# Kernel optimization log

Measured on AMD Instinct MI355X. Metric: run time of the kernel, lower is better.

Reference implementation:

```python
import jax, jax.numpy as jnp
import numpy as np

N = 100_000      # nodes
E = 1_600_000    # directed edges (avg degree 16)
IN_C, HID, LAT, L = 128, 64, 32, 3


def setup_inputs() -> dict:
    key = jax.random.key(0)
    ks = jax.random.split(key, 12)
    s = 0.05
    x = jax.random.normal(ks[0], (N, IN_C), dtype=jnp.float32)
    edge_index = jax.random.randint(ks[1], (2, E), 0, N, dtype=jnp.int32)
    W_in = jax.random.normal(ks[2], (IN_C, HID), dtype=jnp.float32) * s
    b_in = jnp.zeros((HID,), jnp.float32)
    Wg = jax.random.normal(ks[3], (L, HID, HID), dtype=jnp.float32) * s
    bg = jnp.zeros((L, HID), jnp.float32)
    Ws = jax.random.normal(ks[4], (L, HID, LAT), dtype=jnp.float32) * s
    bs = jnp.zeros((L, LAT), jnp.float32)
    Wl = jax.random.normal(ks[5], (HID, LAT), dtype=jnp.float32) * s
    bl = jnp.zeros((LAT,), jnp.float32)
    return {"x": x, "edge_index": edge_index, "W_in": W_in, "b_in": b_in,
            "Wg": Wg, "bg": bg, "Ws": Ws, "bs": bs, "Wl": Wl, "bl": bl}


def reference(x, edge_index, W_in, b_in, Wg, bg, Ws, bs, Wl, bl):
    # --- GCN normalization (PyG GCNConv: add self-loops, sym deg norm) ---
    src, dst = edge_index[0], edge_index[1]
    loops = jnp.arange(N, dtype=src.dtype)
    src_f = jnp.concatenate([src, loops])   # [E+N]
    dst_f = jnp.concatenate([dst, loops])
    deg = jax.ops.segment_sum(jnp.ones(E + N, x.dtype), dst_f, num_segments=N)
    dinv = jnp.where(deg > 0, jax.lax.rsqrt(deg), 0.0)
    norm = (dinv[src_f] * dinv[dst_f])[:, None]  # [E+N, 1]

    def gcn(h, W, b):
        hw = h @ W                                   # [N, out]
        msg = hw[src_f] * norm                       # gather + scale
        return jax.ops.segment_sum(msg, dst_f, num_segments=N) + b

    h = x @ W_in + b_in
    skips = []
    for i in range(L):
        skips.append(h)
        h = jax.nn.leaky_relu(gcn(h, Wg[i], bg[i]), negative_slope=0.2)
        # dropout(p=0.01) is identity in eval mode
    latent = gcn(h, Wl, bl)
    for i in range(L):
        latent = latent + skips[i] @ Ws[i] + bs[i]
    return latent
```

## Files before the change

kernel.cpp:

```cpp
#include <hip/hip_runtime.h>


#define HID 64
#define LAT 32
#define PW 128

static inline int cdiv(long long a, long long b) { return (int)((a + b - 1) / b); }


__global__ __launch_bounds__(256) void hist_kernel(const int* __restrict__ dst,
                                                   int* __restrict__ hist,
                                                   int E, int nb1, int chunk) {
    __shared__ int h[1024];
    int w = blockIdx.x, t = threadIdx.x;
    for (int i = t; i < nb1; i += 256) h[i] = 0;
    __syncthreads();
    int beg = w * chunk, end = min(E, beg + chunk);
    for (int e = beg + t; e < end; e += 256) atomicAdd(&h[dst[e] >> 7], 1);
    __syncthreads();
    for (int i = t; i < nb1; i += 256) hist[i * PW + w] = h[i];
}

__global__ __launch_bounds__(PW) void colscan_kernel(const int* __restrict__ hist,
                                                     int* __restrict__ colprefix,
                                                     int* __restrict__ btot) {
    __shared__ int s[PW];
    int b = blockIdx.x, t = threadIdx.x;
    int v = hist[b * PW + t];
    s[t] = v;
    __syncthreads();
    for (int off = 1; off < PW; off <<= 1) {
        int x = (t >= off) ? s[t - off] : 0;
        __syncthreads();
        s[t] += x;
        __syncthreads();
    }
    colprefix[b * PW + t] = s[t] - v;
    if (t == PW - 1) btot[b] = s[t];
}

__global__ __launch_bounds__(1024) void bscan_kernel(const int* __restrict__ btot,
                                                     int* __restrict__ bstart, int nb1, int E) {
    __shared__ int s[1024];
    int t = threadIdx.x;
    int v = (t < nb1) ? btot[t] : 0;
    s[t] = v;
    __syncthreads();
    for (int off = 1; off < 1024; off <<= 1) {
        int x = (t >= off) ? s[t - off] : 0;
        __syncthreads();
        s[t] += x;
        __syncthreads();
    }
    if (t < nb1) bstart[t] = s[t] - v;
    if (t == 0) bstart[nb1] = E;
}

__global__ __launch_bounds__(256) void partition_kernel(
        const int* __restrict__ src, const int* __restrict__ dst,
        const int* __restrict__ bstart, const int* __restrict__ colprefix,
        unsigned* __restrict__ bbuf, int E, int nb1, int chunk) {
    __shared__ int cur[1024];
    int w = blockIdx.x, t = threadIdx.x;
    for (int i = t; i < nb1; i += 256) cur[i] = bstart[i] + colprefix[i * PW + w];
    __syncthreads();
    int beg = w * chunk, end = min(E, beg + chunk);
    for (int e = beg + t; e < end; e += 256) {
        int s = src[e], d = dst[e];
        int pos = atomicAdd(&cur[d >> 7], 1);
        bbuf[pos] = ((unsigned)(d & 127) << 17) | (unsigned)s;
    }
}

__global__ __launch_bounds__(256) void build_csr_kernel(
        const int* __restrict__ bstart, const unsigned* __restrict__ bbuf,
        int* __restrict__ csr, int* __restrict__ rowstart, float* __restrict__ dinv,
        int n, int E) {
    __shared__ int lcount[128], lpre[128], lcur[128];
    int b = blockIdx.x, t = threadIdx.x;
    int bst = bstart[b], bend = bstart[b + 1];

    if (t < 128) lcount[t] = 0;
    __syncthreads();
    for (int i = bst + t; i < bend; i += 256) atomicAdd(&lcount[bbuf[i] >> 17], 1);
    __syncthreads();
    if (t == 0) {
        int run = 0;
        for (int k = 0; k < 128; ++k) {
            lpre[k] = run;
            lcur[k] = run;
            run += lcount[k];
        }
    }
    __syncthreads();
    if (t < 128) {
        int v = (b << 7) + t;
        if (v < n) {
            rowstart[v] = bst + lpre[t];
            dinv[v] = rsqrtf((float)(lcount[t] + 1));
        }
    }
    if (b == 0 && t == 0) rowstart[n] = E;
    for (int i = bst + t; i < bend; i += 256) {
        unsigned p = bbuf[i];
        int pos = bst + atomicAdd(&lcur[p >> 17], 1);
        csr[pos] = (int)(p & 0x1FFFFu);
    }
}


__global__ __launch_bounds__(256) void input_fused_kernel(
        const float* __restrict__ x, const float* __restrict__ Win,
        const float* __restrict__ bin, const float* __restrict__ Wg0,
        const float* __restrict__ Ws0, const float* __restrict__ dinv,
        const float* __restrict__ bl, const float* __restrict__ bs,
        float* __restrict__ hw, float* __restrict__ out, int n) {
    __shared__ float h0[64 * 68];
    int t = threadIdx.x;
    int vbase = blockIdx.x * 64;
    int rg = t >> 4, lc = t & 15;

    int r0 = vbase + rg * 4;
    const float* xp0 = x + (size_t)(r0 + 0 < n ? r0 + 0 : n - 1) * 128;
    const float* xp1 = x + (size_t)(r0 + 1 < n ? r0 + 1 : n - 1) * 128;
    const float* xp2 = x + (size_t)(r0 + 2 < n ? r0 + 2 : n - 1) * 128;
    const float* xp3 = x + (size_t)(r0 + 3 < n ? r0 + 3 : n - 1) * 128;

    {
        float4 b4 = *(const float4*)&bin[4 * lc];
        float4 a0 = b4, a1 = b4, a2 = b4, a3 = b4;
#pragma unroll 4
        for (int k = 0; k < 128; k += 4) {
            float4 x0 = *(const float4*)&xp0[k];
            float4 x1 = *(const float4*)&xp1[k];
            float4 x2 = *(const float4*)&xp2[k];
            float4 x3 = *(const float4*)&xp3[k];
            float4 w;
            w = *(const float4*)&Win[(k + 0) * 64 + 4 * lc];
            a0.x = fmaf(x0.x, w.x, a0.x); a0.y = fmaf(x0.x, w.y, a0.y);
            a0.z = fmaf(x0.x, w.z, a0.z); a0.w = fmaf(x0.x, w.w, a0.w);
            a1.x = fmaf(x1.x, w.x, a1.x); a1.y = fmaf(x1.x, w.y, a1.y);
            a1.z = fmaf(x1.x, w.z, a1.z); a1.w = fmaf(x1.x, w.w, a1.w);
            a2.x = fmaf(x2.x, w.x, a2.x); a2.y = fmaf(x2.x, w.y, a2.y);
            a2.z = fmaf(x2.x, w.z, a2.z); a2.w = fmaf(x2.x, w.w, a2.w);
            a3.x = fmaf(x3.x, w.x, a3.x); a3.y = fmaf(x3.x, w.y, a3.y);
            a3.z = fmaf(x3.x, w.z, a3.z); a3.w = fmaf(x3.x, w.w, a3.w);
            w = *(const float4*)&Win[(k + 1) * 64 + 4 * lc];
            a0.x = fmaf(x0.y, w.x, a0.x); a0.y = fmaf(x0.y, w.y, a0.y);
            a0.z = fmaf(x0.y, w.z, a0.z); a0.w = fmaf(x0.y, w.w, a0.w);
            a1.x = fmaf(x1.y, w.x, a1.x); a1.y = fmaf(x1.y, w.y, a1.y);
            a1.z = fmaf(x1.y, w.z, a1.z); a1.w = fmaf(x1.y, w.w, a1.w);
            a2.x = fmaf(x2.y, w.x, a2.x); a2.y = fmaf(x2.y, w.y, a2.y);
            a2.z = fmaf(x2.y, w.z, a2.z); a2.w = fmaf(x2.y, w.w, a2.w);
            a3.x = fmaf(x3.y, w.x, a3.x); a3.y = fmaf(x3.y, w.y, a3.y);
            a3.z = fmaf(x3.y, w.z, a3.z); a3.w = fmaf(x3.y, w.w, a3.w);
            w = *(const float4*)&Win[(k + 2) * 64 + 4 * lc];
            a0.x = fmaf(x0.z, w.x, a0.x); a0.y = fmaf(x0.z, w.y, a0.y);
            a0.z = fmaf(x0.z, w.z, a0.z); a0.w = fmaf(x0.z, w.w, a0.w);
            a1.x = fmaf(x1.z, w.x, a1.x); a1.y = fmaf(x1.z, w.y, a1.y);
            a1.z = fmaf(x1.z, w.z, a1.z); a1.w = fmaf(x1.z, w.w, a1.w);
            a2.x = fmaf(x2.z, w.x, a2.x); a2.y = fmaf(x2.z, w.y, a2.y);
            a2.z = fmaf(x2.z, w.z, a2.z); a2.w = fmaf(x2.z, w.w, a2.w);
            a3.x = fmaf(x3.z, w.x, a3.x); a3.y = fmaf(x3.z, w.y, a3.y);
            a3.z = fmaf(x3.z, w.z, a3.z); a3.w = fmaf(x3.z, w.w, a3.w);
            w = *(const float4*)&Win[(k + 3) * 64 + 4 * lc];
            a0.x = fmaf(x0.w, w.x, a0.x); a0.y = fmaf(x0.w, w.y, a0.y);
            a0.z = fmaf(x0.w, w.z, a0.z); a0.w = fmaf(x0.w, w.w, a0.w);
            a1.x = fmaf(x1.w, w.x, a1.x); a1.y = fmaf(x1.w, w.y, a1.y);
            a1.z = fmaf(x1.w, w.z, a1.z); a1.w = fmaf(x1.w, w.w, a1.w);
            a2.x = fmaf(x2.w, w.x, a2.x); a2.y = fmaf(x2.w, w.y, a2.y);
            a2.z = fmaf(x2.w, w.z, a2.z); a2.w = fmaf(x2.w, w.w, a2.w);
            a3.x = fmaf(x3.w, w.x, a3.x); a3.y = fmaf(x3.w, w.y, a3.y);
            a3.z = fmaf(x3.w, w.z, a3.z); a3.w = fmaf(x3.w, w.w, a3.w);
        }
        *(float4*)&h0[(rg * 4 + 0) * 68 + 4 * lc] = a0;
        *(float4*)&h0[(rg * 4 + 1) * 68 + 4 * lc] = a1;
        *(float4*)&h0[(rg * 4 + 2) * 68 + 4 * lc] = a2;
        *(float4*)&h0[(rg * 4 + 3) * 68 + 4 * lc] = a3;
    }
    __syncthreads();

    {
        float4 a0, a1, a2, a3;
        a0 = a1 = a2 = a3 = make_float4(0.f, 0.f, 0.f, 0.f);
#pragma unroll 8
        for (int k = 0; k < 64; ++k) {
            float4 w = *(const float4*)&Wg0[k * 64 + 4 * lc];
            float x0 = h0[(rg * 4 + 0) * 68 + k];
            float x1 = h0[(rg * 4 + 1) * 68 + k];
            float x2 = h0[(rg * 4 + 2) * 68 + k];
            float x3 = h0[(rg * 4 + 3) * 68 + k];
            a0.x = fmaf(x0, w.x, a0.x); a0.y = fmaf(x0, w.y, a0.y);
            a0.z = fmaf(x0, w.z, a0.z); a0.w = fmaf(x0, w.w, a0.w);
            a1.x = fmaf(x1, w.x, a1.x); a1.y = fmaf(x1, w.y, a1.y);
            a1.z = fmaf(x1, w.z, a1.z); a1.w = fmaf(x1, w.w, a1.w);
            a2.x = fmaf(x2, w.x, a2.x); a2.y = fmaf(x2, w.y, a2.y);
            a2.z = fmaf(x2, w.z, a2.z); a2.w = fmaf(x2, w.w, a2.w);
            a3.x = fmaf(x3, w.x, a3.x); a3.y = fmaf(x3, w.y, a3.y);
            a3.z = fmaf(x3, w.z, a3.z); a3.w = fmaf(x3, w.w, a3.w);
        }
#pragma unroll
        for (int r = 0; r < 4; ++r) {
            int v = vbase + rg * 4 + r;
            if (v < n) {
                float di = dinv[v];
                float4 a = (r == 0) ? a0 : (r == 1) ? a1 : (r == 2) ? a2 : a3;
                a.x *= di; a.y *= di; a.z *= di; a.w *= di;
                *(float4*)&hw[(size_t)v * 64 + 4 * lc] = a;
            }
        }
    }

    {
        int sg = t >> 3, sc = t & 7;
        float4 bb = *(const float4*)&bl[4 * sc];
        float4 q0 = *(const float4*)&bs[4 * sc];
        float4 q1 = *(const float4*)&bs[LAT + 4 * sc];
        float4 q2 = *(const float4*)&bs[2 * LAT + 4 * sc];
        bb.x += q0.x + q1.x + q2.x; bb.y += q0.y + q1.y + q2.y;
        bb.z += q0.z + q1.z + q2.z; bb.w += q0.w + q1.w + q2.w;
        float4 a0 = bb, a1 = bb;
#pragma unroll 8
        for (int k = 0; k < 64; ++k) {
            float4 w = *(const float4*)&Ws0[k * 32 + 4 * sc];
            float x0 = h0[(sg * 2 + 0) * 68 + k];
            float x1 = h0[(sg * 2 + 1) * 68 + k];
            a0.x = fmaf(x0, w.x, a0.x); a0.y = fmaf(x0, w.y, a0.y);
            a0.z = fmaf(x0, w.z, a0.z); a0.w = fmaf(x0, w.w, a0.w);
            a1.x = fmaf(x1, w.x, a1.x); a1.y = fmaf(x1, w.y, a1.y);
            a1.z = fmaf(x1, w.z, a1.z); a1.w = fmaf(x1, w.w, a1.w);
        }
#pragma unroll
        for (int r = 0; r < 2; ++r) {
            int v = vbase + sg * 2 + r;
            if (v < n)
                *(float4*)&out[(size_t)v * 32 + 4 * sc] = (r == 0) ? a0 : a1;
        }
    }
}


template <bool LAST>
__global__ __launch_bounds__(256) void gather_transform_kernel(
        const int* __restrict__ rowstart, const int* __restrict__ csr,
        const float* __restrict__ dinv, const float* __restrict__ hwin,
        const float* __restrict__ bias, const float* __restrict__ Wg,
        const float* __restrict__ Ws, float* __restrict__ hwout,
        float* __restrict__ out, int n) {
    __shared__ float hL[64 * 68];
    int t = threadIdx.x;
    int vbase = blockIdx.x * 64;
    int ns = t >> 4, lc = t & 15;

    float4 b4 = *(const float4*)&bias[4 * lc];
#pragma unroll
    for (int b = 0; b < 4; ++b) {
        int row = b * 16 + ns;
        int v = vbase + row;
        if (v < n) {
            int beg = rowstart[v];
            int end = rowstart[v + 1];
            float di = dinv[v];
            float4 acc = *(const float4*)&hwin[(size_t)v * 64 + 4 * lc];
            const float* base = hwin + 4 * lc;
            int e = beg;
            for (; e + 3 < end; e += 4) {
                int s0 = csr[e], s1 = csr[e + 1], s2 = csr[e + 2], s3 = csr[e + 3];
                float4 g0 = *(const float4*)&base[(size_t)s0 * 64];
                float4 g1 = *(const float4*)&base[(size_t)s1 * 64];
                float4 g2 = *(const float4*)&base[(size_t)s2 * 64];
                float4 g3 = *(const float4*)&base[(size_t)s3 * 64];
                acc.x += (g0.x + g1.x) + (g2.x + g3.x);
                acc.y += (g0.y + g1.y) + (g2.y + g3.y);
                acc.z += (g0.z + g1.z) + (g2.z + g3.z);
                acc.w += (g0.w + g1.w) + (g2.w + g3.w);
            }
            for (; e < end; ++e) {
                float4 g0 = *(const float4*)&base[(size_t)csr[e] * 64];
                acc.x += g0.x; acc.y += g0.y; acc.z += g0.z; acc.w += g0.w;
            }
            float4 h;
            h.x = di * acc.x + b4.x; h.x = h.x > 0.f ? h.x : 0.2f * h.x;
            h.y = di * acc.y + b4.y; h.y = h.y > 0.f ? h.y : 0.2f * h.y;
            h.z = di * acc.z + b4.z; h.z = h.z > 0.f ? h.z : 0.2f * h.z;
            h.w = di * acc.w + b4.w; h.w = h.w > 0.f ? h.w : 0.2f * h.w;
            *(float4*)&hL[row * 68 + 4 * lc] = h;
        }
    }
    __syncthreads();

    if (!LAST) {
        int rg = t >> 4;
        float4 a0, a1, a2, a3;
        a0 = a1 = a2 = a3 = make_float4(0.f, 0.f, 0.f, 0.f);
#pragma unroll 8
        for (int k = 0; k < 64; ++k) {
            float4 w = *(const float4*)&Wg[k * 64 + 4 * lc];
            float x0 = hL[(rg * 4 + 0) * 68 + k];
            float x1 = hL[(rg * 4 + 1) * 68 + k];
            float x2 = hL[(rg * 4 + 2) * 68 + k];
            float x3 = hL[(rg * 4 + 3) * 68 + k];
            a0.x = fmaf(x0, w.x, a0.x); a0.y = fmaf(x0, w.y, a0.y);
            a0.z = fmaf(x0, w.z, a0.z); a0.w = fmaf(x0, w.w, a0.w);
            a1.x = fmaf(x1, w.x, a1.x); a1.y = fmaf(x1, w.y, a1.y);
            a1.z = fmaf(x1, w.z, a1.z); a1.w = fmaf(x1, w.w, a1.w);
            a2.x = fmaf(x2, w.x, a2.x); a2.y = fmaf(x2, w.y, a2.y);
            a2.z = fmaf(x2, w.z, a2.z); a2.w = fmaf(x2, w.w, a2.w);
            a3.x = fmaf(x3, w.x, a3.x); a3.y = fmaf(x3, w.y, a3.y);
            a3.z = fmaf(x3, w.z, a3.z); a3.w = fmaf(x3, w.w, a3.w);
        }
#pragma unroll
        for (int r = 0; r < 4; ++r) {
            int v = vbase + rg * 4 + r;
            if (v < n) {
                float di = dinv[v];
                float4 a = (r == 0) ? a0 : (r == 1) ? a1 : (r == 2) ? a2 : a3;
                a.x *= di; a.y *= di; a.z *= di; a.w *= di;
                *(float4*)&hwout[(size_t)v * 64 + 4 * lc] = a;
            }
        }

        int sg = t >> 3, sc = t & 7;
        float4 s0, s1;
        s0 = s1 = make_float4(0.f, 0.f, 0.f, 0.f);
#pragma unroll 8
        for (int k = 0; k < 64; ++k) {
            float4 w = *(const float4*)&Ws[k * 32 + 4 * sc];
            float x0 = hL[(sg * 2 + 0) * 68 + k];
            float x1 = hL[(sg * 2 + 1) * 68 + k];
            s0.x = fmaf(x0, w.x, s0.x); s0.y = fmaf(x0, w.y, s0.y);
            s0.z = fmaf(x0, w.z, s0.z); s0.w = fmaf(x0, w.w, s0.w);
            s1.x = fmaf(x1, w.x, s1.x); s1.y = fmaf(x1, w.y, s1.y);
            s1.z = fmaf(x1, w.z, s1.z); s1.w = fmaf(x1, w.w, s1.w);
        }
#pragma unroll
        for (int r = 0; r < 2; ++r) {
            int v = vbase + sg * 2 + r;
            if (v < n) {
                float4 a = (r == 0) ? s0 : s1;
                float4* op = (float4*)(out + (size_t)v * 32 + 4 * sc);
                float4 o = *op;
                o.x += a.x; o.y += a.y; o.z += a.z; o.w += a.w;
                *op = o;
            }
        }
    } else {
        int sg = t >> 3, sc = t & 7;
        float4 s0, s1;
        s0 = s1 = make_float4(0.f, 0.f, 0.f, 0.f);
#pragma unroll 8
        for (int k = 0; k < 64; ++k) {
            float4 w = *(const float4*)&Ws[k * 32 + 4 * sc];
            float x0 = hL[(sg * 2 + 0) * 68 + k];
            float x1 = hL[(sg * 2 + 1) * 68 + k];
            s0.x = fmaf(x0, w.x, s0.x); s0.y = fmaf(x0, w.y, s0.y);
            s0.z = fmaf(x0, w.z, s0.z); s0.w = fmaf(x0, w.w, s0.w);
            s1.x = fmaf(x1, w.x, s1.x); s1.y = fmaf(x1, w.y, s1.y);
            s1.z = fmaf(x1, w.z, s1.z); s1.w = fmaf(x1, w.w, s1.w);
        }
#pragma unroll
        for (int r = 0; r < 2; ++r) {
            int v = vbase + sg * 2 + r;
            if (v < n) {
                float di = dinv[v];
                float4 a = (r == 0) ? s0 : s1;
                a.x *= di; a.y *= di; a.z *= di; a.w *= di;
                *(float4*)&hwout[(size_t)v * 32 + 4 * sc] = a;
            }
        }
    }
}


__global__ __launch_bounds__(256) void gather_out_kernel(
        const int* __restrict__ rowstart, const int* __restrict__ csr,
        const float* __restrict__ dinv, const float* __restrict__ hwl,
        float* __restrict__ out, int n) {
    int t = threadIdx.x;
    int lr = t >> 3, lc = t & 7;
    int v = blockIdx.x * 32 + lr;
    if (v >= n) return;
    int beg = rowstart[v], end = rowstart[v + 1];
    float4 acc = *(const float4*)&hwl[(size_t)v * 32 + 4 * lc];
    const float* base = hwl + 4 * lc;
    int e = beg;
    for (; e + 3 < end; e += 4) {
        int s0 = csr[e], s1 = csr[e + 1], s2 = csr[e + 2], s3 = csr[e + 3];
        float4 a0 = *(const float4*)&base[(size_t)s0 * 32];
        float4 a1 = *(const float4*)&base[(size_t)s1 * 32];
        float4 a2 = *(const float4*)&base[(size_t)s2 * 32];
        float4 a3 = *(const float4*)&base[(size_t)s3 * 32];
        acc.x += (a0.x + a1.x) + (a2.x + a3.x);
        acc.y += (a0.y + a1.y) + (a2.y + a3.y);
        acc.z += (a0.z + a1.z) + (a2.z + a3.z);
        acc.w += (a0.w + a1.w) + (a2.w + a3.w);
    }
    for (; e < end; ++e) {
        float4 a0 = *(const float4*)&base[(size_t)csr[e] * 32];
        acc.x += a0.x; acc.y += a0.y; acc.z += a0.z; acc.w += a0.w;
    }
    float di = dinv[v];
    float4* op = (float4*)(out + (size_t)v * 32 + 4 * lc);
    float4 o = *op;
    o.x += di * acc.x; o.y += di * acc.y; o.z += di * acc.z; o.w += di * acc.w;
    *op = o;
}


extern "C" void kernel_launch(void* const* d_in, const int* in_sizes, int n_in,
                              void* d_out, int out_size, void* d_ws, size_t ws_size,
                              hipStream_t stream) {
    const float* x    = (const float*)d_in[0];
    const int*   ei   = (const int*)d_in[1];
    const float* W_in = (const float*)d_in[2];
    const float* b_in = (const float*)d_in[3];
    const float* Wg   = (const float*)d_in[4];
    const float* bg   = (const float*)d_in[5];
    const float* Ws   = (const float*)d_in[6];
    const float* bs   = (const float*)d_in[7];
    const float* Wl   = (const float*)d_in[8];
    const float* bl   = (const float*)d_in[9];

    const int N = in_sizes[0] / 128;
    const int E = in_sizes[1] / 2;
    const int nb1 = cdiv(N, 128);
    const int chunk = cdiv(E, PW);
    const int* srcp = ei;
    const int* dstp = ei + E;

    char* p = (char*)d_ws;
    float*    hwA      = (float*)p;    p += (size_t)N * HID * 4;
    float*    hwB      = (float*)p;    p += (size_t)N * HID * 4;
    unsigned* bbuf     = (unsigned*)p; p += (size_t)E * 4;
    int*      csr      = (int*)p;      p += (size_t)E * 4;
    int*      rowstart = (int*)p;      p += ((size_t)N + 1) * 4;
    float*    dinv     = (float*)p;    p += (size_t)N * 4;
    int*      hist     = (int*)p;      p += (size_t)nb1 * PW * 4;
    int*      colpre   = (int*)p;      p += (size_t)nb1 * PW * 4;
    int*      btot     = (int*)p;      p += (size_t)nb1 * 4;
    int*      bstart   = (int*)p;      p += ((size_t)nb1 + 1) * 4;
    float*    out      = (float*)d_out;

    const int B = 256;

    hist_kernel<<<PW, B, 0, stream>>>(dstp, hist, E, nb1, chunk);
    colscan_kernel<<<nb1, PW, 0, stream>>>(hist, colpre, btot);
    bscan_kernel<<<1, 1024, 0, stream>>>(btot, bstart, nb1, E);
    partition_kernel<<<PW, B, 0, stream>>>(srcp, dstp, bstart, colpre, bbuf, E, nb1, chunk);
    build_csr_kernel<<<nb1, B, 0, stream>>>(bstart, bbuf, csr, rowstart, dinv, N, E);

    input_fused_kernel<<<cdiv(N, 64), B, 0, stream>>>(
        x, W_in, b_in, Wg, Ws, dinv, bl, bs, hwA, out, N);

    gather_transform_kernel<false><<<cdiv(N, 64), B, 0, stream>>>(
        rowstart, csr, dinv, hwA, bg, Wg + 4096, Ws + 2048, hwB, out, N);

    gather_transform_kernel<false><<<cdiv(N, 64), B, 0, stream>>>(
        rowstart, csr, dinv, hwB, bg + 64, Wg + 8192, Ws + 4096, hwA, out, N);

    gather_transform_kernel<true><<<cdiv(N, 64), B, 0, stream>>>(
        rowstart, csr, dinv, hwA, bg + 128, nullptr, Wl, hwB, nullptr, N);

    gather_out_kernel<<<cdiv(N, 32), B, 0, stream>>>(rowstart, csr, dinv, hwB, out, N);
}
```

Before: 513.3 us.

## Pad CSR rows to multiples of 8 with dummy zero node; stage x tiles in LDS

Each bucket's CSR segment is given a fixed capacity (CCAP per 128 destination nodes) and every row is padded to a multiple of 8 with a sentinel index n, whose feature row is zeroed. Gather loops then load neighbour indices as int4 pairs and run 8-wide with no remainder loop. The input GEMM also now stages x through double-buffered shared memory in 32-column chunks instead of reading x rows directly per thread. The padding wastes gather bandwidth on zero rows, and the fixed CCAP capacity assumes no 128-node bucket exceeds about 3456 padded edges, which could overflow on skewed graphs.

```diff
diff --git a/kernel.cpp b/kernel.cpp
--- a/kernel.cpp
+++ b/kernel.cpp
@@ -4,6 +4,7 @@
 #define HID 64
 #define LAT 32
 #define PW 128
+#define CCAP 3456
 
 static inline int cdiv(long long a, long long b) { return (int)((a + b - 1) / b); }
 
@@ -74,11 +75,12 @@
 
 __global__ __launch_bounds__(256) void build_csr_kernel(
         const int* __restrict__ bstart, const unsigned* __restrict__ bbuf,
-        int* __restrict__ csr, int* __restrict__ rowstart, float* __restrict__ dinv,
-        int n, int E) {
+        int* __restrict__ csr, int* __restrict__ rowbeg, int* __restrict__ rowend,
+        float* __restrict__ dinv, int n) {
     __shared__ int lcount[128], lpre[128], lcur[128];
     int b = blockIdx.x, t = threadIdx.x;
     int bst = bstart[b], bend = bstart[b + 1];
+    int base = b * CCAP;
 
     if (t < 128) lcount[t] = 0;
     __syncthreads();
@@ -89,22 +91,29 @@
         for (int k = 0; k < 128; ++k) {
             lpre[k] = run;
             lcur[k] = run;
-            run += lcount[k];
+            run += (lcount[k] + 7) & ~7;
         }
     }
     __syncthreads();
     if (t < 128) {
         int v = (b << 7) + t;
         if (v < n) {
-            rowstart[v] = bst + lpre[t];
+            int beg = base + lpre[t];
+            rowbeg[v] = beg;
+            rowend[v] = beg + ((lcount[t] + 7) & ~7);
             dinv[v] = rsqrtf((float)(lcount[t] + 1));
         }
     }
-    if (b == 0 && t == 0) rowstart[n] = E;
     for (int i = bst + t; i < bend; i += 256) {
         unsigned p = bbuf[i];
-        int pos = bst + atomicAdd(&lcur[p >> 17], 1);
+        int pos = base + atomicAdd(&lcur[p >> 17], 1);
         csr[pos] = (int)(p & 0x1FFFFu);
+    }
+    __syncthreads();
+    if (t < 128) {
+        int s = base + lpre[t] + lcount[t];
+        int epad = base + lpre[t] + ((lcount[t] + 7) & ~7);
+        for (int i = s; i < epad; ++i) csr[i] = n;
     }
 }
 
@@ -115,81 +124,43 @@
         const float* __restrict__ Ws0, const float* __restrict__ dinv,
         const float* __restrict__ bl, const float* __restrict__ bs,
         float* __restrict__ hw, float* __restrict__ out, int n) {
+    __shared__ float xs[2][64 * 33];
     __shared__ float h0[64 * 68];
     int t = threadIdx.x;
     int vbase = blockIdx.x * 64;
     int rg = t >> 4, lc = t & 15;
 
-    int r0 = vbase + rg * 4;
-    const float* xp0 = x + (size_t)(r0 + 0 < n ? r0 + 0 : n - 1) * 128;
-    const float* xp1 = x + (size_t)(r0 + 1 < n ? r0 + 1 : n - 1) * 128;
-    const float* xp2 = x + (size_t)(r0 + 2 < n ? r0 + 2 : n - 1) * 128;
-    const float* xp3 = x + (size_t)(r0 + 3 < n ? r0 + 3 : n - 1) * 128;
-
-    {
-        float4 b4 = *(const float4*)&bin[4 * lc];
-        float4 a0 = b4, a1 = b4, a2 = b4, a3 = b4;
-#pragma unroll 4
-        for (int k = 0; k < 128; k += 4) {
-            float4 x0 = *(const float4*)&xp0[k];
-            float4 x1 = *(const float4*)&xp1[k];
-            float4 x2 = *(const float4*)&xp2[k];
-            float4 x3 = *(const float4*)&xp3[k];
-            float4 w;
-            w = *(const float4*)&Win[(k + 0) * 64 + 4 * lc];
-            a0.x = fmaf(x0.x, w.x, a0.x); a0.y = fmaf(x0.x, w.y, a0.y);
-            a0.z = fmaf(x0.x, w.z, a0.z); a0.w = fmaf(x0.x, w.w, a0.w);
-            a1.x = fmaf(x1.x, w.x, a1.x); a1.y = fmaf(x1.x, w.y, a1.y);
-            a1.z = fmaf(x1.x, w.z, a1.z); a1.w = fmaf(x1.x, w.w, a1.w);
-            a2.x = fmaf(x2.x, w.x, a2.x); a2.y = fmaf(x2.x, w.y, a2.y);
-            a2.z = fmaf(x2.x, w.z, a2.z); a2.w = fmaf(x2.x, w.w, a2.w);
-            a3.x = fmaf(x3.x, w.x, a3.x); a3.y = fmaf(x3.x, w.y, a3.y);
-            a3.z = fmaf(x3.x, w.z, a3.z); a3.w = fmaf(x3.x, w.w, a3.w);
-            w = *(const float4*)&Win[(k + 1) * 64 + 4 * lc];
-            a0.x = fmaf(x0.y, w.x, a0.x); a0.y = fmaf(x0.y, w.y, a0.y);
-            a0.z = fmaf(x0.y, w.z, a0.z); a0.w = fmaf(x0.y, w.w, a0.w);
-            a1.x = fmaf(x1.y, w.x, a1.x); a1.y = fmaf(x1.y, w.y, a1.y);
-            a1.z = fmaf(x1.y, w.z, a1.z); a1.w = fmaf(x1.y, w.w, a1.w);
-            a2.x = fmaf(x2.y, w.x, a2.x); a2.y = fmaf(x2.y, w.y, a2.y);
-            a2.z = fmaf(x2.y, w.z, a2.z); a2.w = fmaf(x2.y, w.w, a2.w);
-            a3.x = fmaf(x3.y, w.x, a3.x); a3.y = fmaf(x3.y, w.y, a3.y);
-            a3.z = fmaf(x3.y, w.z, a3.z); a3.w = fmaf(x3.y, w.w, a3.w);
-            w = *(const float4*)&Win[(k + 2) * 64 + 4 * lc];
-            a0.x = fmaf(x0.z, w.x, a0.x); a0.y = fmaf(x0.z, w.y, a0.y);
-            a0.z = fmaf(x0.z, w.z, a0.z); a0.w = fmaf(x0.z, w.w, a0.w);
-            a1.x = fmaf(x1.z, w.x, a1.x); a1.y = fmaf(x1.z, w.y, a1.y);
-            a1.z = fmaf(x1.z, w.z, a1.z); a1.w = fmaf(x1.z, w.w, a1.w);
-            a2.x = fmaf(x2.z, w.x, a2.x); a2.y = fmaf(x2.z, w.y, a2.y);
-            a2.z = fmaf(x2.z, w.z, a2.z); a2.w = fmaf(x2.z, w.w, a2.w);
-            a3.x = fmaf(x3.z, w.x, a3.x); a3.y = fmaf(x3.z, w.y, a3.y);
-            a3.z = fmaf(x3.z, w.z, a3.z); a3.w = fmaf(x3.z, w.w, a3.w);
-            w = *(const float4*)&Win[(k + 3) * 64 + 4 * lc];
-            a0.x = fmaf(x0.w, w.x, a0.x); a0.y = fmaf(x0.w, w.y, a0.y);
-            a0.z = fmaf(x0.w, w.z, a0.z); a0.w = fmaf(x0.w, w.w, a0.w);
-            a1.x = fmaf(x1.w, w.x, a1.x); a1.y = fmaf(x1.w, w.y, a1.y);
-            a1.z = fmaf(x1.w, w.z, a1.z); a1.w = fmaf(x1.w, w.w, a1.w);
-            a2.x = fmaf(x2.w, w.x, a2.x); a2.y = fmaf(x2.w, w.y, a2.y);
-            a2.z = fmaf(x2.w, w.z, a2.z); a2.w = fmaf(x2.w, w.w, a2.w);
-            a3.x = fmaf(x3.w, w.x, a3.x); a3.y = fmaf(x3.w, w.y, a3.y);
-            a3.z = fmaf(x3.w, w.z, a3.z); a3.w = fmaf(x3.w, w.w, a3.w);
-        }
-        *(float4*)&h0[(rg * 4 + 0) * 68 + 4 * lc] = a0;
-        *(float4*)&h0[(rg * 4 + 1) * 68 + 4 * lc] = a1;
-        *(float4*)&h0[(rg * 4 + 2) * 68 + 4 * lc] = a2;
-        *(float4*)&h0[(rg * 4 + 3) * 68 + 4 * lc] = a3;
-    }
-    __syncthreads();
-
-    {
-        float4 a0, a1, a2, a3;
-        a0 = a1 = a2 = a3 = make_float4(0.f, 0.f, 0.f, 0.f);
-#pragma unroll 8
-        for (int k = 0; k < 64; ++k) {
-            float4 w = *(const float4*)&Wg0[k * 64 + 4 * lc];
-            float x0 = h0[(rg * 4 + 0) * 68 + k];
-            float x1 = h0[(rg * 4 + 1) * 68 + k];
-            float x2 = h0[(rg * 4 + 2) * 68 + k];
-            float x3 = h0[(rg * 4 + 3) * 68 + k];
+    if (blockIdx.x == 0 && t < 64) hw[(size_t)n * 64 + t] = 0.f;
+
+    int srow = t >> 3, scol = (t & 7) * 4;
+    long long gr0 = vbase + srow;      if (gr0 >= n) gr0 = n - 1;
+    long long gr1 = vbase + srow + 32; if (gr1 >= n) gr1 = n - 1;
+    const float* gp0 = x + gr0 * 128 + scol;
+    const float* gp1 = x + gr1 * 128 + scol;
+
+    float4 p0 = *(const float4*)&gp0[0];
+    float4 p1 = *(const float4*)&gp1[0];
+    *(float4*)&xs[0][srow * 33 + scol] = p0;
+    *(float4*)&xs[0][(srow + 32) * 33 + scol] = p1;
+    __syncthreads();
+
+    float4 b4 = *(const float4*)&bin[4 * lc];
+    float4 a0 = b4, a1 = b4, a2 = b4, a3 = b4;
+#pragma unroll
+    for (int c = 0; c < 4; ++c) {
+        if (c < 3) {
+            p0 = *(const float4*)&gp0[(c + 1) * 32];
+            p1 = *(const float4*)&gp1[(c + 1) * 32];
+        }
+        const float* xb = xs[c & 1];
+        const float* wb = Win + (size_t)c * 32 * 64;
+#pragma unroll
+        for (int kk = 0; kk < 32; ++kk) {
+            float4 w = *(const float4*)&wb[kk * 64 + 4 * lc];
+            float x0 = xb[(rg * 4 + 0) * 33 + kk];
+            float x1 = xb[(rg * 4 + 1) * 33 + kk];
+            float x2 = xb[(rg * 4 + 2) * 33 + kk];
+            float x3 = xb[(rg * 4 + 3) * 33 + kk];
             a0.x = fmaf(x0, w.x, a0.x); a0.y = fmaf(x0, w.y, a0.y);
             a0.z = fmaf(x0, w.z, a0.z); a0.w = fmaf(x0, w.w, a0.w);
             a1.x = fmaf(x1, w.x, a1.x); a1.y = fmaf(x1, w.y, a1.y);
@@ -199,12 +170,43 @@
             a3.x = fmaf(x3, w.x, a3.x); a3.y = fmaf(x3, w.y, a3.y);
             a3.z = fmaf(x3, w.z, a3.z); a3.w = fmaf(x3, w.w, a3.w);
         }
+        if (c < 3) {
+            *(float4*)&xs[(c + 1) & 1][srow * 33 + scol] = p0;
+            *(float4*)&xs[(c + 1) & 1][(srow + 32) * 33 + scol] = p1;
+            __syncthreads();
+        }
+    }
+    *(float4*)&h0[(rg * 4 + 0) * 68 + 4 * lc] = a0;
+    *(float4*)&h0[(rg * 4 + 1) * 68 + 4 * lc] = a1;
+    *(float4*)&h0[(rg * 4 + 2) * 68 + 4 * lc] = a2;
+    *(float4*)&h0[(rg * 4 + 3) * 68 + 4 * lc] = a3;
+    __syncthreads();
+
+    {
+        float4 c0, c1, c2, c3;
+        c0 = c1 = c2 = c3 = make_float4(0.f, 0.f, 0.f, 0.f);
+#pragma unroll 8
+        for (int k = 0; k < 64; ++k) {
+            float4 w = *(const float4*)&Wg0[k * 64 + 4 * lc];
+            float x0 = h0[(rg * 4 + 0) * 68 + k];
+            float x1 = h0[(rg * 4 + 1) * 68 + k];
+            float x2 = h0[(rg * 4 + 2) * 68 + k];
+            float x3 = h0[(rg * 4 + 3) * 68 + k];
+            c0.x = fmaf(x0, w.x, c0.x); c0.y = fmaf(x0, w.y, c0.y);
+            c0.z = fmaf(x0, w.z, c0.z); c0.w = fmaf(x0, w.w, c0.w);
+            c1.x = fmaf(x1, w.x, c1.x); c1.y = fmaf(x1, w.y, c1.y);
+            c1.z = fmaf(x1, w.z, c1.z); c1.w = fmaf(x1, w.w, c1.w);
+            c2.x = fmaf(x2, w.x, c2.x); c2.y = fmaf(x2, w.y, c2.y);
+            c2.z = fmaf(x2, w.z, c2.z); c2.w = fmaf(x2, w.w, c2.w);
+            c3.x = fmaf(x3, w.x, c3.x); c3.y = fmaf(x3, w.y, c3.y);
+            c3.z = fmaf(x3, w.z, c3.z); c3.w = fmaf(x3, w.w, c3.w);
+        }
 #pragma unroll
         for (int r = 0; r < 4; ++r) {
             int v = vbase + rg * 4 + r;
             if (v < n) {
                 float di = dinv[v];
-                float4 a = (r == 0) ? a0 : (r == 1) ? a1 : (r == 2) ? a2 : a3;
+                float4 a = (r == 0) ? c0 : (r == 1) ? c1 : (r == 2) ? c2 : c3;
                 a.x *= di; a.y *= di; a.z *= di; a.w *= di;
                 *(float4*)&hw[(size_t)v * 64 + 4 * lc] = a;
             }
@@ -219,22 +221,22 @@
         float4 q2 = *(const float4*)&bs[2 * LAT + 4 * sc];
         bb.x += q0.x + q1.x + q2.x; bb.y += q0.y + q1.y + q2.y;
         bb.z += q0.z + q1.z + q2.z; bb.w += q0.w + q1.w + q2.w;
-        float4 a0 = bb, a1 = bb;
+        float4 s0 = bb, s1 = bb;
 #pragma unroll 8
         for (int k = 0; k < 64; ++k) {
             float4 w = *(const float4*)&Ws0[k * 32 + 4 * sc];
             float x0 = h0[(sg * 2 + 0) * 68 + k];
             float x1 = h0[(sg * 2 + 1) * 68 + k];
-            a0.x = fmaf(x0, w.x, a0.x); a0.y = fmaf(x0, w.y, a0.y);
-            a0.z = fmaf(x0, w.z, a0.z); a0.w = fmaf(x0, w.w, a0.w);
-            a1.x = fmaf(x1, w.x, a1.x); a1.y = fmaf(x1, w.y, a1.y);
-            a1.z = fmaf(x1, w.z, a1.z); a1.w = fmaf(x1, w.w, a1.w);
+            s0.x = fmaf(x0, w.x, s0.x); s0.y = fmaf(x0, w.y, s0.y);
+            s0.z = fmaf(x0, w.z, s0.z); s0.w = fmaf(x0, w.w, s0.w);
+            s1.x = fmaf(x1, w.x, s1.x); s1.y = fmaf(x1, w.y, s1.y);
+            s1.z = fmaf(x1, w.z, s1.z); s1.w = fmaf(x1, w.w, s1.w);
         }
 #pragma unroll
         for (int r = 0; r < 2; ++r) {
             int v = vbase + sg * 2 + r;
             if (v < n)
-                *(float4*)&out[(size_t)v * 32 + 4 * sc] = (r == 0) ? a0 : a1;
+                *(float4*)&out[(size_t)v * 32 + 4 * sc] = (r == 0) ? s0 : s1;
         }
     }
 }
@@ -242,42 +244,46 @@
 
 template <bool LAST>
 __global__ __launch_bounds__(256) void gather_transform_kernel(
-        const int* __restrict__ rowstart, const int* __restrict__ csr,
-        const float* __restrict__ dinv, const float* __restrict__ hwin,
-        const float* __restrict__ bias, const float* __restrict__ Wg,
-        const float* __restrict__ Ws, float* __restrict__ hwout,
-        float* __restrict__ out, int n) {
+        const int* __restrict__ rowbeg, const int* __restrict__ rowend,
+        const int* __restrict__ csr, const float* __restrict__ dinv,
+        const float* __restrict__ hwin, const float* __restrict__ bias,
+        const float* __restrict__ Wg, const float* __restrict__ Ws,
+        float* __restrict__ hwout, float* __restrict__ out, int n) {
     __shared__ float hL[64 * 68];
     int t = threadIdx.x;
     int vbase = blockIdx.x * 64;
     int ns = t >> 4, lc = t & 15;
 
+    if (blockIdx.x == 0) {
+        if (!LAST) { if (t < 64) hwout[(size_t)n * 64 + t] = 0.f; }
+        else       { if (t < 32) hwout[(size_t)n * 32 + t] = 0.f; }
+    }
+
     float4 b4 = *(const float4*)&bias[4 * lc];
 #pragma unroll
     for (int b = 0; b < 4; ++b) {
         int row = b * 16 + ns;
         int v = vbase + row;
         if (v < n) {
-            int beg = rowstart[v];
-            int end = rowstart[v + 1];
+            int beg = rowbeg[v], end = rowend[v];
             float di = dinv[v];
             float4 acc = *(const float4*)&hwin[(size_t)v * 64 + 4 * lc];
             const float* base = hwin + 4 * lc;
-            int e = beg;
-            for (; e + 3 < end; e += 4) {
-                int s0 = csr[e], s1 = csr[e + 1], s2 = csr[e + 2], s3 = csr[e + 3];
-                float4 g0 = *(const float4*)&base[(size_t)s0 * 64];
-                float4 g1 = *(const float4*)&base[(size_t)s1 * 64];
-                float4 g2 = *(const float4*)&base[(size_t)s2 * 64];
-                float4 g3 = *(const float4*)&base[(size_t)s3 * 64];
-                acc.x += (g0.x + g1.x) + (g2.x + g3.x);
-                acc.y += (g0.y + g1.y) + (g2.y + g3.y);
-                acc.z += (g0.z + g1.z) + (g2.z + g3.z);
-                acc.w += (g0.w + g1.w) + (g2.w + g3.w);
-            }
-            for (; e < end; ++e) {
-                float4 g0 = *(const float4*)&base[(size_t)csr[e] * 64];
-                acc.x += g0.x; acc.y += g0.y; acc.z += g0.z; acc.w += g0.w;
+            for (int e = beg; e < end; e += 8) {
+                int4 ca = *(const int4*)&csr[e];
+                int4 cb = *(const int4*)&csr[e + 4];
+                float4 g0 = *(const float4*)&base[(size_t)ca.x * 64];
+                float4 g1 = *(const float4*)&base[(size_t)ca.y * 64];
+                float4 g2 = *(const float4*)&base[(size_t)ca.z * 64];
+                float4 g3 = *(const float4*)&base[(size_t)ca.w * 64];
+                float4 g4 = *(const float4*)&base[(size_t)cb.x * 64];
+                float4 g5 = *(const float4*)&base[(size_t)cb.y * 64];
+                float4 g6 = *(const float4*)&base[(size_t)cb.z * 64];
+                float4 g7 = *(const float4*)&base[(size_t)cb.w * 64];
+                acc.x += ((g0.x + g1.x) + (g2.x + g3.x)) + ((g4.x + g5.x) + (g6.x + g7.x));
+                acc.y += ((g0.y + g1.y) + (g2.y + g3.y)) + ((g4.y + g5.y) + (g6.y + g7.y));
+                acc.z += ((g0.z + g1.z) + (g2.z + g3.z)) + ((g4.z + g5.z) + (g6.z + g7.z));
+                acc.w += ((g0.w + g1.w) + (g2.w + g3.w)) + ((g4.w + g5.w) + (g6.w + g7.w));
             }
             float4 h;
             h.x = di * acc.x + b4.x; h.x = h.x > 0.f ? h.x : 0.2f * h.x;
@@ -291,8 +297,8 @@
 
     if (!LAST) {
         int rg = t >> 4;
-        float4 a0, a1, a2, a3;
-        a0 = a1 = a2 = a3 = make_float4(0.f, 0.f, 0.f, 0.f);
+        float4 c0, c1, c2, c3;
+        c0 = c1 = c2 = c3 = make_float4(0.f, 0.f, 0.f, 0.f);
 #pragma unroll 8
         for (int k = 0; k < 64; ++k) {
             float4 w = *(const float4*)&Wg[k * 64 + 4 * lc];
@@ -300,21 +306,21 @@
             float x1 = hL[(rg * 4 + 1) * 68 + k];
             float x2 = hL[(rg * 4 + 2) * 68 + k];
             float x3 = hL[(rg * 4 + 3) * 68 + k];
-            a0.x = fmaf(x0, w.x, a0.x); a0.y = fmaf(x0, w.y, a0.y);
-            a0.z = fmaf(x0, w.z, a0.z); a0.w = fmaf(x0, w.w, a0.w);
-            a1.x = fmaf(x1, w.x, a1.x); a1.y = fmaf(x1, w.y, a1.y);
-            a1.z = fmaf(x1, w.z, a1.z); a1.w = fmaf(x1, w.w, a1.w);
-            a2.x = fmaf(x2, w.x, a2.x); a2.y = fmaf(x2, w.y, a2.y);
-            a2.z = fmaf(x2, w.z, a2.z); a2.w = fmaf(x2, w.w, a2.w);
-            a3.x = fmaf(x3, w.x, a3.x); a3.y = fmaf(x3, w.y, a3.y);
-            a3.z = fmaf(x3, w.z, a3.z); a3.w = fmaf(x3, w.w, a3.w);
+            c0.x = fmaf(x0, w.x, c0.x); c0.y = fmaf(x0, w.y, c0.y);
+            c0.z = fmaf(x0, w.z, c0.z); c0.w = fmaf(x0, w.w, c0.w);
+            c1.x = fmaf(x1, w.x, c1.x); c1.y = fmaf(x1, w.y, c1.y);
+            c1.z = fmaf(x1, w.z, c1.z); c1.w = fmaf(x1, w.w, c1.w);
+            c2.x = fmaf(x2, w.x, c2.x); c2.y = fmaf(x2, w.y, c2.y);
+            c2.z = fmaf(x2, w.z, c2.z); c2.w = fmaf(x2, w.w, c2.w);
+            c3.x = fmaf(x3, w.x, c3.x); c3.y = fmaf(x3, w.y, c3.y);
+            c3.z = fmaf(x3, w.z, c3.z); c3.w = fmaf(x3, w.w, c3.w);
         }
 #pragma unroll
         for (int r = 0; r < 4; ++r) {
             int v = vbase + rg * 4 + r;
             if (v < n) {
                 float di = dinv[v];
-                float4 a = (r == 0) ? a0 : (r == 1) ? a1 : (r == 2) ? a2 : a3;
+                float4 a = (r == 0) ? c0 : (r == 1) ? c1 : (r == 2) ? c2 : c3;
                 a.x *= di; a.y *= di; a.z *= di; a.w *= di;
                 *(float4*)&hwout[(size_t)v * 64 + 4 * lc] = a;
             }
@@ -373,31 +379,31 @@
 
 
 __global__ __launch_bounds__(256) void gather_out_kernel(
-        const int* __restrict__ rowstart, const int* __restrict__ csr,
-        const float* __restrict__ dinv, const float* __restrict__ hwl,
-        float* __restrict__ out, int n) {
+        const int* __restrict__ rowbeg, const int* __restrict__ rowend,
+        const int* __restrict__ csr, const float* __restrict__ dinv,
+        const float* __restrict__ hwl, float* __restrict__ out, int n) {
     int t = threadIdx.x;
     int lr = t >> 3, lc = t & 7;
     int v = blockIdx.x * 32 + lr;
     if (v >= n) return;
-    int beg = rowstart[v], end = rowstart[v + 1];
+    int beg = rowbeg[v], end = rowend[v];
     float4 acc = *(const float4*)&hwl[(size_t)v * 32 + 4 * lc];
     const float* base = hwl + 4 * lc;
-    int e = beg;
-    for (; e + 3 < end; e += 4) {
-        int s0 = csr[e], s1 = csr[e + 1], s2 = csr[e + 2], s3 = csr[e + 3];
-        float4 a0 = *(const float4*)&base[(size_t)s0 * 32];
-        float4 a1 = *(const float4*)&base[(size_t)s1 * 32];
-        float4 a2 = *(const float4*)&base[(size_t)s2 * 32];
-        float4 a3 = *(const float4*)&base[(size_t)s3 * 32];
-        acc.x += (a0.x + a1.x) + (a2.x + a3.x);
-        acc.y += (a0.y + a1.y) + (a2.y + a3.y);
-        acc.z += (a0.z + a1.z) + (a2.z + a3.z);
-        acc.w += (a0.w + a1.w) + (a2.w + a3.w);
-    }
-    for (; e < end; ++e) {
-        float4 a0 = *(const float4*)&base[(size_t)csr[e] * 32];
-        acc.x += a0.x; acc.y += a0.y; acc.z += a0.z; acc.w += a0.w;
+    for (int e = beg; e < end; e += 8) {
+        int4 ca = *(const int4*)&csr[e];
+        int4 cb = *(const int4*)&csr[e + 4];
+        float4 g0 = *(const float4*)&base[(size_t)ca.x * 32];
+        float4 g1 = *(const float4*)&base[(size_t)ca.y * 32];
+        float4 g2 = *(const float4*)&base[(size_t)ca.z * 32];
+        float4 g3 = *(const float4*)&base[(size_t)ca.w * 32];
+        float4 g4 = *(const float4*)&base[(size_t)cb.x * 32];
+        float4 g5 = *(const float4*)&base[(size_t)cb.y * 32];
+        float4 g6 = *(const float4*)&base[(size_t)cb.z * 32];
+        float4 g7 = *(const float4*)&base[(size_t)cb.w * 32];
+        acc.x += ((g0.x + g1.x) + (g2.x + g3.x)) + ((g4.x + g5.x) + (g6.x + g7.x));
+        acc.y += ((g0.y + g1.y) + (g2.y + g3.y)) + ((g4.y + g5.y) + (g6.y + g7.y));
+        acc.z += ((g0.z + g1.z) + (g2.z + g3.z)) + ((g4.z + g5.z) + (g6.z + g7.z));
+        acc.w += ((g0.w + g1.w) + (g2.w + g3.w)) + ((g4.w + g5.w) + (g6.w + g7.w));
     }
     float di = dinv[v];
     float4* op = (float4*)(out + (size_t)v * 32 + 4 * lc);
@@ -429,11 +435,12 @@
     const int* dstp = ei + E;
 
     char* p = (char*)d_ws;
-    float*    hwA      = (float*)p;    p += (size_t)N * HID * 4;
-    float*    hwB      = (float*)p;    p += (size_t)N * HID * 4;
+    float*    hwA      = (float*)p;    p += ((size_t)N + 1) * HID * 4;
+    float*    hwB      = (float*)p;    p += ((size_t)N + 1) * HID * 4;
     unsigned* bbuf     = (unsigned*)p; p += (size_t)E * 4;
-    int*      csr      = (int*)p;      p += (size_t)E * 4;
-    int*      rowstart = (int*)p;      p += ((size_t)N + 1) * 4;
+    int*      csr      = (int*)p;      p += (size_t)nb1 * CCAP * 4;
+    int*      rowbeg   = (int*)p;      p += (size_t)N * 4;
+    int*      rowend   = (int*)p;      p += (size_t)N * 4;
     float*    dinv     = (float*)p;    p += (size_t)N * 4;
     int*      hist     = (int*)p;      p += (size_t)nb1 * PW * 4;
     int*      colpre   = (int*)p;      p += (size_t)nb1 * PW * 4;
@@ -447,19 +454,19 @@
     colscan_kernel<<<nb1, PW, 0, stream>>>(hist, colpre, btot);
     bscan_kernel<<<1, 1024, 0, stream>>>(btot, bstart, nb1, E);
     partition_kernel<<<PW, B, 0, stream>>>(srcp, dstp, bstart, colpre, bbuf, E, nb1, chunk);
-    build_csr_kernel<<<nb1, B, 0, stream>>>(bstart, bbuf, csr, rowstart, dinv, N, E);
+    build_csr_kernel<<<nb1, B, 0, stream>>>(bstart, bbuf, csr, rowbeg, rowend, dinv, N);
 
     input_fused_kernel<<<cdiv(N, 64), B, 0, stream>>>(
         x, W_in, b_in, Wg, Ws, dinv, bl, bs, hwA, out, N);
 
     gather_transform_kernel<false><<<cdiv(N, 64), B, 0, stream>>>(
-        rowstart, csr, dinv, hwA, bg, Wg + 4096, Ws + 2048, hwB, out, N);
+        rowbeg, rowend, csr, dinv, hwA, bg, Wg + 4096, Ws + 2048, hwB, out, N);
 
     gather_transform_kernel<false><<<cdiv(N, 64), B, 0, stream>>>(
-        rowstart, csr, dinv, hwB, bg + 64, Wg + 8192, Ws + 4096, hwA, out, N);
+        rowbeg, rowend, csr, dinv, hwB, bg + 64, Wg + 8192, Ws + 4096, hwA, out, N);
 
     gather_transform_kernel<true><<<cdiv(N, 64), B, 0, stream>>>(
-        rowstart, csr, dinv, hwA, bg + 128, nullptr, Wl, hwB, nullptr, N);
-
-    gather_out_kernel<<<cdiv(N, 32), B, 0, stream>>>(rowstart, csr, dinv, hwB, out, N);
-}
+        rowbeg, rowend, csr, dinv, hwA, bg + 128, nullptr, Wl, hwB, nullptr, N);
+
+    gather_out_kernel<<<cdiv(N, 32), B, 0, stream>>>(rowbeg, rowend, csr, dinv, hwB, out, N);
+}
```

Result: faster. 491.6 us (-4.2%).
